# Kernel optimization log

Hardware: AMD Instinct MI355X
Metric: run time of the kernel (lower is better)

Reference implementation:

```python
import jax, jax.numpy as jnp
import numpy as np

TEMP = 0.05
EPS = 1e-8  # matches torch F.cosine_similarity eps default


def setup_inputs() -> dict:
    key = jax.random.key(0)
    k1, k2 = jax.random.split(key)
    B, L, H = 2048, 13, 768
    cls = jax.random.normal(k1, (B, H), dtype=jnp.float32)
    hidden = jax.random.normal(k2, (B, L, H), dtype=jnp.float32)
    return {"cls": cls, "hidden": hidden}


def _normalize(x, axis=-1):
    n = jnp.sqrt(jnp.sum(x * x, axis=axis, keepdims=True))
    return x / jnp.maximum(n, EPS)


def reference(cls, hidden):
    B, L, H = hidden.shape
    cn = _normalize(cls)            # [B, H]
    hn = _normalize(hidden)         # [B, L, H]

    # exp(cos(cls_i, hidden_{i,k}) / temp) -- aligned (diagonal) similarities
    sim_ci_hik = jnp.exp(jnp.einsum('id,ild->il', cn, hn) / TEMP)  # [B, L]

    # exp(cos(cls_i, hidden_{m,n}) / temp) -- all pairs, flattened (m,n)-major
    sim_ci_hmn = jnp.exp(jnp.einsum('id,mnd->imn', cn, hn) / TEMP)  # [B, B, L]
    sim_flat = sim_ci_hmn.reshape(B, B * L)                         # [B, B*L]

    # faithful to original: mask tiles (1 - eye(B)) L times along columns,
    # i.e. zeroes columns c with c % B == i (layout quirk of the source code)
    hmn_mask = jnp.tile(1.0 - jnp.eye(B, dtype=sim_flat.dtype), (1, L))  # [B, B*L]
    s = jnp.sum(sim_flat * hmn_mask, axis=1)                             # [B]

    loss = jnp.mean(-jnp.log(sim_ci_hik) + jnp.log(sim_ci_hik + s[:, None]))
    return loss
```

## Files before the change

### kernel.cpp

```cpp
#include <hip/hip_runtime.h>
#include <cstdint>
#include <cstddef>

#define B_    2048
#define L_    13
#define H_    768
#define NROW  (B_ * L_)
#define RTEMP 20.0f
#define NT    12
#define RS    768
#define NTILE 3328

typedef float f32x4 __attribute__((ext_vector_type(4)));
typedef long  i64x2 __attribute__((ext_vector_type(2)));

static __device__ __forceinline__ unsigned int f2e4m3(float f) {
  unsigned int u = __float_as_uint(f);
  unsigned int s = (u >> 24) & 0x80u;
  unsigned int ua = u & 0x7fffffffu;
  if (ua >= 0x43e80000u) return s | 0x7eu;
  if (ua < 0x3c800000u) {
    int m = (int)rintf(__uint_as_float(ua) * 512.0f);
    return s | (unsigned int)m;
  }
  unsigned int lsb = (ua >> 20) & 1u;
  unsigned int r = ua + 0x7ffffu + lsb;
  int Ee = (int)((r >> 23) & 0xffu) - 127;
  unsigned int mant = (r >> 20) & 7u;
  return s | (unsigned int)(((Ee + 7) << 3) | mant);
}

__device__ __forceinline__ void llds16(const void* g, void* l) {
  __builtin_amdgcn_global_load_lds(
      (const __attribute__((address_space(1))) void*)g,
      (__attribute__((address_space(3))) void*)l, 16, 0, 0);
}

#define BAR do { asm volatile("" ::: "memory");            \
    __builtin_amdgcn_s_barrier();                          \
    asm volatile("" ::: "memory"); } while (0)

#define OFF8(k) ((((k) >> 6) << 6) + (((((k) & 31) >> 3)) << 4) + ((((k) & 32) ? 8 : 0)) + ((k) & 7))

__global__ __launch_bounds__(256) void k_normalize(
    const float* __restrict__ cls, const float* __restrict__ hidden,
    unsigned char* __restrict__ cn8, unsigned char* __restrict__ hn8,
    float* __restrict__ S_all, float* __restrict__ out)
{
  if (blockIdx.x == 0) {
#pragma unroll
    for (int i = 0; i < 8; ++i) S_all[threadIdx.x * 8 + i] = 0.0f;
    if (threadIdx.x == 0) *out = 0.0f;
  }

  const int wid = threadIdx.x >> 6, lane = threadIdx.x & 63;
  const int row = blockIdx.x * 4 + wid;
  const float4* src; unsigned char* dst;
  if (row < B_) { src = (const float4*)(cls + (size_t)row * H_);           dst = cn8 + (size_t)row * RS; }
  else          { src = (const float4*)(hidden + (size_t)(row - B_) * H_); dst = hn8 + (size_t)(row - B_) * RS; }

  float4 x0 = src[lane], x1 = src[lane + 64], x2 = src[lane + 128];
  float ss = x0.x*x0.x + x0.y*x0.y + x0.z*x0.z + x0.w*x0.w
           + x1.x*x1.x + x1.y*x1.y + x1.z*x1.z + x1.w*x1.w
           + x2.x*x2.x + x2.y*x2.y + x2.z*x2.z + x2.w*x2.w;
#pragma unroll
  for (int m = 1; m < 64; m <<= 1) ss += __shfl_xor(ss, m);
  const float sc = 1.0f / fmaxf(sqrtf(ss), 1e-8f);

  const int k = lane * 4;
  unsigned int p0 = f2e4m3(x0.x*sc) | (f2e4m3(x0.y*sc) << 8) | (f2e4m3(x0.z*sc) << 16) | (f2e4m3(x0.w*sc) << 24);
  unsigned int p1 = f2e4m3(x1.x*sc) | (f2e4m3(x1.y*sc) << 8) | (f2e4m3(x1.z*sc) << 16) | (f2e4m3(x1.w*sc) << 24);
  unsigned int p2 = f2e4m3(x2.x*sc) | (f2e4m3(x2.y*sc) << 8) | (f2e4m3(x2.z*sc) << 16) | (f2e4m3(x2.w*sc) << 24);
  *(unsigned int*)(dst + OFF8(k))       = p0;
  *(unsigned int*)(dst + OFF8(k + 256)) = p1;
  *(unsigned int*)(dst + OFF8(k + 512)) = p2;
}

__global__ __launch_bounds__(256, 4) void k_gemm(
    const unsigned char* __restrict__ cn8,
    const unsigned char* __restrict__ hn8,
    float* __restrict__ S_all,
    float* __restrict__ alignedD)
{
  __shared__ __align__(16) char lds[40960];

  const int tid  = threadIdx.x;
  const int lane = tid & 63;
  const int wid  = tid >> 6;
  const int wm   = wid >> 1;
  const int wn   = wid & 1;
  const int fr   = lane & 15, q = lane >> 4, fr2 = (lane & 15) >> 1;

  const int swz  = ((q | ((fr & 1) << 2)) ^ (fr2 & 7)) << 4;
  const int offA = wm * 4096 + fr2 * 128 + swz;
  const int offB = wn * 4096 + fr2 * 128 + swz;

  const int slot_un = (tid & 7) ^ ((tid >> 3) & 7);
  const int srow = 2 * (tid >> 3) + (slot_un >> 2);
  const int scb  = (slot_un & 3) << 4;
  char* ldst = lds + tid * 16;

  const int tile = blockIdx.x;
  const int xcd  = tile & 7;
  const int idx  = tile >> 3;
  const int brow = (idx & 15) << 7;
  const int bcol = (xcd * 26 + (idx >> 4)) << 7;

  const char* gA = (const char*)cn8 + (size_t)(brow + srow) * RS + scb;
  const char* gB = (const char*)hn8 + (size_t)(bcol + srow) * RS + scb;

#define STAGE_A(sb, t) do {                                       \
    char* d_ = ldst + (sb);                                       \
    const char* a_ = gA + (t) * 64;                               \
    llds16(a_,           d_);                                     \
    llds16(a_ + 64 * RS, d_ + 4096);                              \
  } while (0)
#define STAGE_B(sb, t) do {                                       \
    char* d_ = ldst + (sb);                                       \
    const char* b_ = gB + (t) * 64;                               \
    llds16(b_,           d_);                                     \
    llds16(b_ + 64 * RS, d_ + 4096);                              \
  } while (0)

  STAGE_A(0, 0);
  STAGE_B(16384, 0);
  STAGE_B(16384 + 8192, 1);
  asm volatile("s_waitcnt vmcnt(2)" ::: "memory");
  BAR;

  f32x4 acc[4][4] = {};

  for (int t = 0; t < NT; ++t) {
    const char* bA = lds + (t & 1) * 8192;
    const char* bB = lds + 16384 + (t % 3) * 8192;

    i64x2 av[4], bv[4];
#pragma unroll
    for (int i = 0; i < 4; ++i) av[i] = *(const i64x2*)(bA + offA + i * 1024);
#pragma unroll
    for (int i = 0; i < 4; ++i) bv[i] = *(const i64x2*)(bB + offB + i * 1024);

    if (t + 1 < NT) STAGE_A(((t + 1) & 1) * 8192, t + 1);
    if (t + 2 < NT) STAGE_B(16384 + ((t + 2) % 3) * 8192, t + 2);

    __builtin_amdgcn_s_setprio(1);
#pragma unroll
    for (int mi = 0; mi < 4; ++mi)
#pragma unroll
      for (int ni = 0; ni < 4; ++ni)
        acc[mi][ni] = __builtin_amdgcn_mfma_f32_16x16x32_fp8_fp8(
            av[mi][0], bv[ni][0], acc[mi][ni], 0, 0, 0);
#pragma unroll
    for (int mi = 0; mi < 4; ++mi)
#pragma unroll
      for (int ni = 0; ni < 4; ++ni)
        acc[mi][ni] = __builtin_amdgcn_mfma_f32_16x16x32_fp8_fp8(
            av[mi][1], bv[ni][1], acc[mi][ni], 0, 0, 0);
    __builtin_amdgcn_s_setprio(0);

    if (t + 2 < NT)      { asm volatile("s_waitcnt vmcnt(2)" ::: "memory"); BAR; }
    else if (t + 1 < NT) { asm volatile("s_waitcnt vmcnt(0)" ::: "memory"); BAR; }
  }
#undef STAGE_A
#undef STAGE_B

  const int rowb = brow + wm * 64;
  const int colb = bcol + wn * 64;
#pragma unroll
  for (int mi = 0; mi < 4; ++mi) {
#pragma unroll
    for (int j = 0; j < 4; ++j) {
      const int grow = rowb + mi * 16 + q * 4 + j;
      float v = 0.f;
#pragma unroll
      for (int ni = 0; ni < 4; ++ni) {
        const int gcol = colb + ni * 16 + fr;
        const float a = acc[mi][ni][j];
        if ((unsigned)(gcol - grow * 13) < 13u) alignedD[gcol] = a;
        v += ((gcol & 2047) == grow) ? 0.f : __expf(RTEMP * a);
      }
      v += __shfl_xor(v, 1); v += __shfl_xor(v, 2);
      v += __shfl_xor(v, 4); v += __shfl_xor(v, 8);
      if (fr == 0) atomicAdd(&S_all[grow], v);
    }
  }
}

__global__ __launch_bounds__(256) void k_finalize(
    const float* __restrict__ S_all, const float* __restrict__ alignedD,
    float* __restrict__ out)
{
  const int i = blockIdx.x * 256 + threadIdx.x;
  const int lane = threadIdx.x & 63, wid = threadIdx.x >> 6;
  const float s = S_all[i];
  float accv = 0.f;
#pragma unroll
  for (int l = 0; l < L_; l++) {
    const float d = RTEMP * alignedD[i * L_ + l];
    accv += logf(__expf(d) + s) - d;
  }
#pragma unroll
  for (int m = 1; m < 64; m <<= 1) accv += __shfl_xor(accv, m);
  __shared__ float wsum[4];
  if (lane == 0) wsum[wid] = accv;
  __syncthreads();
  if (threadIdx.x == 0)
    atomicAdd(out, (wsum[0] + wsum[1] + wsum[2] + wsum[3]) * (1.0f / (float)(B_ * L_)));
}

extern "C" void kernel_launch(void* const* d_in, const int* in_sizes, int n_in,
                              void* d_out, int out_size, void* d_ws, size_t ws_size,
                              hipStream_t stream) {
  const float* cls    = (const float*)d_in[0];
  const float* hidden = (const float*)d_in[1];
  float* out = (float*)d_out;

  char* ws = (char*)d_ws;
  unsigned char* hn8 = (unsigned char*)ws;
  unsigned char* cn8 = (unsigned char*)(ws + (size_t)NROW * RS);
  float* S_all    = (float*)(ws + (size_t)NROW * RS + (size_t)B_ * RS);
  float* alignedD = (float*)(ws + (size_t)NROW * RS + (size_t)B_ * RS + B_ * sizeof(float));

  k_normalize<<<(B_ + NROW) / 4, 256, 0, stream>>>(cls, hidden, cn8, hn8, S_all, out);
  k_gemm<<<NTILE, 256, 0, stream>>>(cn8, hn8, S_all, alignedD);
  k_finalize<<<B_ / 256, 256, 0, stream>>>(S_all, alignedD, out);
}
```

Baseline: 92.15 us.

## Restructure FP8 GEMM main loop into triple-buffered pipeline with register prefetch

Replaces the asymmetric A-double/B-triple LDS buffering with a uniform triple buffer for both operands and a loop unrolled by two. The loop keeps two register fragment sets so LDS reads for the next K-step are issued before the MFMAs of the current one. The aim is to hide LDS read and global-to-LDS load latency behind matrix work. In exchange, LDS per block grows to 48 KB and the occupancy hint drops from 4 to 3 blocks per CU, and every step now waits for vmcnt(0).

```diff
diff --git a/kernel.cpp b/kernel.cpp
--- a/kernel.cpp
+++ b/kernel.cpp
@@ -39,6 +39,7 @@
 #define BAR do { asm volatile("" ::: "memory");            \
     __builtin_amdgcn_s_barrier();                          \
     asm volatile("" ::: "memory"); } while (0)
+#define WAITV0 asm volatile("s_waitcnt vmcnt(0)" ::: "memory")
 
 #define OFF8(k) ((((k) >> 6) << 6) + (((((k) & 31) >> 3)) << 4) + ((((k) & 32) ? 8 : 0)) + ((k) & 7))
 
@@ -76,13 +77,13 @@
   *(unsigned int*)(dst + OFF8(k + 512)) = p2;
 }
 
-__global__ __launch_bounds__(256, 4) void k_gemm(
+__global__ __launch_bounds__(256, 3) void k_gemm(
     const unsigned char* __restrict__ cn8,
     const unsigned char* __restrict__ hn8,
     float* __restrict__ S_all,
     float* __restrict__ alignedD)
 {
-  __shared__ __align__(16) char lds[40960];
+  __shared__ __align__(16) char lds[49152];
 
   const int tid  = threadIdx.x;
   const int lane = tid & 63;
@@ -98,7 +99,6 @@
   const int slot_un = (tid & 7) ^ ((tid >> 3) & 7);
   const int srow = 2 * (tid >> 3) + (slot_un >> 2);
   const int scb  = (slot_un & 3) << 4;
-  char* ldst = lds + tid * 16;
 
   const int tile = blockIdx.x;
   const int xcd  = tile & 7;
@@ -109,60 +109,84 @@
   const char* gA = (const char*)cn8 + (size_t)(brow + srow) * RS + scb;
   const char* gB = (const char*)hn8 + (size_t)(bcol + srow) * RS + scb;
 
-#define STAGE_A(sb, t) do {                                       \
-    char* d_ = ldst + (sb);                                       \
+  char* aCur = lds;          char* bCur = lds + 24576;
+  char* aNxt = lds + 8192;   char* bNxt = lds + 32768;
+  char* aWr  = lds + 16384;  char* bWr  = lds + 40960;
+
+#define STAGE(pa, pb, t) do {                                     \
     const char* a_ = gA + (t) * 64;                               \
-    llds16(a_,           d_);                                     \
-    llds16(a_ + 64 * RS, d_ + 4096);                              \
+    llds16(a_,           (pa) + tid * 16);                        \
+    llds16(a_ + 64 * RS, (pa) + 4096 + tid * 16);                 \
+    const char* b_ = gB + (t) * 64;                               \
+    llds16(b_,           (pb) + tid * 16);                        \
+    llds16(b_ + 64 * RS, (pb) + 4096 + tid * 16);                 \
   } while (0)
-#define STAGE_B(sb, t) do {                                       \
-    char* d_ = ldst + (sb);                                       \
-    const char* b_ = gB + (t) * 64;                               \
-    llds16(b_,           d_);                                     \
-    llds16(b_ + 64 * RS, d_ + 4096);                              \
+
+#define READSET(av, bv, pa, pb) do {                              \
+    _Pragma("unroll")                                             \
+    for (int i = 0; i < 4; ++i)                                   \
+      av[i] = *(const i64x2*)((pa) + offA + i * 1024);            \
+    _Pragma("unroll")                                             \
+    for (int i = 0; i < 4; ++i)                                   \
+      bv[i] = *(const i64x2*)((pb) + offB + i * 1024);            \
   } while (0)
 
-  STAGE_A(0, 0);
-  STAGE_B(16384, 0);
-  STAGE_B(16384 + 8192, 1);
-  asm volatile("s_waitcnt vmcnt(2)" ::: "memory");
+#define MFMAS(av, bv) do {                                        \
+    __builtin_amdgcn_s_setprio(1);                                \
+    _Pragma("unroll")                                             \
+    for (int mi = 0; mi < 4; ++mi)                                \
+      _Pragma("unroll")                                           \
+      for (int ni = 0; ni < 4; ++ni)                              \
+        acc[mi][ni] = __builtin_amdgcn_mfma_f32_16x16x32_fp8_fp8( \
+            av[mi][0], bv[ni][0], acc[mi][ni], 0, 0, 0);          \
+    _Pragma("unroll")                                             \
+    for (int mi = 0; mi < 4; ++mi)                                \
+      _Pragma("unroll")                                           \
+      for (int ni = 0; ni < 4; ++ni)                              \
+        acc[mi][ni] = __builtin_amdgcn_mfma_f32_16x16x32_fp8_fp8( \
+            av[mi][1], bv[ni][1], acc[mi][ni], 0, 0, 0);          \
+    __builtin_amdgcn_s_setprio(0);                                \
+  } while (0)
+
+#define ROTATE do { char* t_;                                     \
+    t_ = aCur; aCur = aNxt; aNxt = aWr; aWr = t_;                 \
+    t_ = bCur; bCur = bNxt; bNxt = bWr; bWr = t_; } while (0)
+
+  f32x4 acc[4][4] = {};
+  i64x2 a0[4], b0[4], a1[4], b1[4];
+
+  STAGE(aCur, bCur, 0);
+  WAITV0;
   BAR;
-
-  f32x4 acc[4][4] = {};
-
-  for (int t = 0; t < NT; ++t) {
-    const char* bA = lds + (t & 1) * 8192;
-    const char* bB = lds + 16384 + (t % 3) * 8192;
-
-    i64x2 av[4], bv[4];
-#pragma unroll
-    for (int i = 0; i < 4; ++i) av[i] = *(const i64x2*)(bA + offA + i * 1024);
-#pragma unroll
-    for (int i = 0; i < 4; ++i) bv[i] = *(const i64x2*)(bB + offB + i * 1024);
-
-    if (t + 1 < NT) STAGE_A(((t + 1) & 1) * 8192, t + 1);
-    if (t + 2 < NT) STAGE_B(16384 + ((t + 2) % 3) * 8192, t + 2);
-
-    __builtin_amdgcn_s_setprio(1);
-#pragma unroll
-    for (int mi = 0; mi < 4; ++mi)
-#pragma unroll
-      for (int ni = 0; ni < 4; ++ni)
-        acc[mi][ni] = __builtin_amdgcn_mfma_f32_16x16x32_fp8_fp8(
-            av[mi][0], bv[ni][0], acc[mi][ni], 0, 0, 0);
-#pragma unroll
-    for (int mi = 0; mi < 4; ++mi)
-#pragma unroll
-      for (int ni = 0; ni < 4; ++ni)
-        acc[mi][ni] = __builtin_amdgcn_mfma_f32_16x16x32_fp8_fp8(
-            av[mi][1], bv[ni][1], acc[mi][ni], 0, 0, 0);
-    __builtin_amdgcn_s_setprio(0);
-
-    if (t + 2 < NT)      { asm volatile("s_waitcnt vmcnt(2)" ::: "memory"); BAR; }
-    else if (t + 1 < NT) { asm volatile("s_waitcnt vmcnt(0)" ::: "memory"); BAR; }
-  }
-#undef STAGE_A
-#undef STAGE_B
+  READSET(a0, b0, aCur, bCur);
+  STAGE(aNxt, bNxt, 1);
+
+  for (int it = 0; it < 5; ++it) {
+    const int t = 2 * it;
+    WAITV0;
+    BAR;
+    READSET(a1, b1, aNxt, bNxt);
+    STAGE(aWr, bWr, t + 2);
+    MFMAS(a0, b0);
+    ROTATE;
+    WAITV0;
+    BAR;
+    READSET(a0, b0, aNxt, bNxt);
+    STAGE(aWr, bWr, t + 3);
+    MFMAS(a1, b1);
+    ROTATE;
+  }
+
+  WAITV0;
+  BAR;
+  READSET(a1, b1, aNxt, bNxt);
+  MFMAS(a0, b0);
+  MFMAS(a1, b1);
+
+#undef STAGE
+#undef READSET
+#undef MFMAS
+#undef ROTATE
 
   const int rowb = brow + wm * 64;
   const int colb = bcol + wn * 64;
```

Result: slower. 114.9 us (+24.6%).

## Restructure fp8 GEMM into a five-stage K=32 LDS ring with a new swizzle

Applied to the files above, without the earlier changes.

The GEMM main loop moves from a K-step of 64, with double-buffered A and triple-buffered B, to a K-step of 32. A and B now share a five-slot LDS ring that keeps up to four stages in flight, and the loop is fully unrolled with explicit vmcnt waits. The normalize kernel stops writing the permuted OFF8 fp8 layout, so a new XOR swizzle for LDS reads and staging addresses replaces it. The aim is deeper latency hiding of global-to-LDS loads. The cost is twice as many barriers and shorter 32-byte contiguous global segments per row.

```diff
diff --git a/kernel.cpp b/kernel.cpp
--- a/kernel.cpp
+++ b/kernel.cpp
@@ -7,12 +7,10 @@
 #define H_    768
 #define NROW  (B_ * L_)
 #define RTEMP 20.0f
-#define NT    12
 #define RS    768
 #define NTILE 3328
 
 typedef float f32x4 __attribute__((ext_vector_type(4)));
-typedef long  i64x2 __attribute__((ext_vector_type(2)));
 
 static __device__ __forceinline__ unsigned int f2e4m3(float f) {
   unsigned int u = __float_as_uint(f);
@@ -40,8 +38,6 @@
     __builtin_amdgcn_s_barrier();                          \
     asm volatile("" ::: "memory"); } while (0)
 
-#define OFF8(k) ((((k) >> 6) << 6) + (((((k) & 31) >> 3)) << 4) + ((((k) & 32) ? 8 : 0)) + ((k) & 7))
-
 __global__ __launch_bounds__(256) void k_normalize(
     const float* __restrict__ cls, const float* __restrict__ hidden,
     unsigned char* __restrict__ cn8, unsigned char* __restrict__ hn8,
@@ -71,9 +67,9 @@
   unsigned int p0 = f2e4m3(x0.x*sc) | (f2e4m3(x0.y*sc) << 8) | (f2e4m3(x0.z*sc) << 16) | (f2e4m3(x0.w*sc) << 24);
   unsigned int p1 = f2e4m3(x1.x*sc) | (f2e4m3(x1.y*sc) << 8) | (f2e4m3(x1.z*sc) << 16) | (f2e4m3(x1.w*sc) << 24);
   unsigned int p2 = f2e4m3(x2.x*sc) | (f2e4m3(x2.y*sc) << 8) | (f2e4m3(x2.z*sc) << 16) | (f2e4m3(x2.w*sc) << 24);
-  *(unsigned int*)(dst + OFF8(k))       = p0;
-  *(unsigned int*)(dst + OFF8(k + 256)) = p1;
-  *(unsigned int*)(dst + OFF8(k + 512)) = p2;
+  *(unsigned int*)(dst + k)       = p0;
+  *(unsigned int*)(dst + k + 256) = p1;
+  *(unsigned int*)(dst + k + 512) = p2;
 }
 
 __global__ __launch_bounds__(256, 4) void k_gemm(
@@ -89,16 +85,29 @@
   const int wid  = tid >> 6;
   const int wm   = wid >> 1;
   const int wn   = wid & 1;
-  const int fr   = lane & 15, q = lane >> 4, fr2 = (lane & 15) >> 1;
-
-  const int swz  = ((q | ((fr & 1) << 2)) ^ (fr2 & 7)) << 4;
-  const int offA = wm * 4096 + fr2 * 128 + swz;
-  const int offB = wn * 4096 + fr2 * 128 + swz;
-
-  const int slot_un = (tid & 7) ^ ((tid >> 3) & 7);
-  const int srow = 2 * (tid >> 3) + (slot_un >> 2);
-  const int scb  = (slot_un & 3) << 4;
-  char* ldst = lds + tid * 16;
+  const int fr   = lane & 15, q = lane >> 4;
+  const int l4   = fr >> 2, c3 = fr & 3;
+
+  int offA[4], offB[4];
+#pragma unroll
+  for (int mi = 0; mi < 4; ++mi) {
+    const int line = wm * 16 + mi * 4 + l4;
+    const int hkey = (mi * 2 + (l4 >> 1)) & 7;
+    const int u    = (c3 * 2 + (q >> 1)) ^ hkey;
+    offA[mi] = line * 128 + u * 16 + (q & 1) * 8;
+  }
+#pragma unroll
+  for (int ni = 0; ni < 4; ++ni) {
+    const int line = wn * 16 + ni * 4 + l4;
+    const int hkey = (ni * 2 + (l4 >> 1)) & 7;
+    const int u    = (c3 * 2 + (q >> 1)) ^ hkey;
+    offB[ni] = 4096 + line * 128 + u * 16 + (q & 1) * 8;
+  }
+
+  const int sline = tid >> 3, su = tid & 7;
+  const int sv    = su ^ ((sline >> 1) & 7);
+  const int srow  = sline * 4 + (sv >> 1);
+  const int skb   = (sv & 1) * 16;
 
   const int tile = blockIdx.x;
   const int xcd  = tile & 7;
@@ -106,63 +115,62 @@
   const int brow = (idx & 15) << 7;
   const int bcol = (xcd * 26 + (idx >> 4)) << 7;
 
-  const char* gA = (const char*)cn8 + (size_t)(brow + srow) * RS + scb;
-  const char* gB = (const char*)hn8 + (size_t)(bcol + srow) * RS + scb;
-
-#define STAGE_A(sb, t) do {                                       \
-    char* d_ = ldst + (sb);                                       \
-    const char* a_ = gA + (t) * 64;                               \
-    llds16(a_,           d_);                                     \
-    llds16(a_ + 64 * RS, d_ + 4096);                              \
+  const char* gA = (const char*)cn8 + (size_t)(brow + srow) * RS + skb;
+  const char* gB = (const char*)hn8 + (size_t)(bcol + srow) * RS + skb;
+  char* dA = lds + tid * 16;
+  char* dB = lds + 4096 + tid * 16;
+
+#define STAGE(slotidx, koff) do {                                 \
+    llds16(gA + (koff), dA + (slotidx) * 8192);                   \
+    llds16(gB + (koff), dB + (slotidx) * 8192);                   \
   } while (0)
-#define STAGE_B(sb, t) do {                                       \
-    char* d_ = ldst + (sb);                                       \
-    const char* b_ = gB + (t) * 64;                               \
-    llds16(b_,           d_);                                     \
-    llds16(b_ + 64 * RS, d_ + 4096);                              \
+
+  f32x4 acc[4][4] = {};
+
+#define DOSTEP(j, stagej, koff, wait) do {                        \
+    if (stagej) STAGE((j + 4) % 5, koff);                         \
+    const char* sb_ = lds + (j) * 8192;                           \
+    long av[4], bv[4];                                            \
+    _Pragma("unroll")                                             \
+    for (int i = 0; i < 4; ++i) av[i] = *(const long*)(sb_ + offA[i]); \
+    _Pragma("unroll")                                             \
+    for (int i = 0; i < 4; ++i) bv[i] = *(const long*)(sb_ + offB[i]); \
+    __builtin_amdgcn_s_setprio(1);                                \
+    _Pragma("unroll")                                             \
+    for (int mi = 0; mi < 4; ++mi)                                \
+      _Pragma("unroll")                                           \
+      for (int ni = 0; ni < 4; ++ni)                              \
+        acc[mi][ni] = __builtin_amdgcn_mfma_f32_16x16x32_fp8_fp8( \
+            av[mi], bv[ni], acc[mi][ni], 0, 0, 0);                \
+    __builtin_amdgcn_s_setprio(0);                                \
+    if (wait >= 0) {                                              \
+      if (wait == 6) asm volatile("s_waitcnt vmcnt(6)" ::: "memory"); \
+      else if (wait == 4) asm volatile("s_waitcnt vmcnt(4)" ::: "memory"); \
+      else if (wait == 2) asm volatile("s_waitcnt vmcnt(2)" ::: "memory"); \
+      else                asm volatile("s_waitcnt vmcnt(0)" ::: "memory"); \
+      BAR;                                                        \
+    }                                                             \
   } while (0)
 
-  STAGE_A(0, 0);
-  STAGE_B(16384, 0);
-  STAGE_B(16384 + 8192, 1);
-  asm volatile("s_waitcnt vmcnt(2)" ::: "memory");
+  STAGE(0, 0); STAGE(1, 32); STAGE(2, 64); STAGE(3, 96);
+  asm volatile("s_waitcnt vmcnt(6)" ::: "memory");
   BAR;
 
-  f32x4 acc[4][4] = {};
-
-  for (int t = 0; t < NT; ++t) {
-    const char* bA = lds + (t & 1) * 8192;
-    const char* bB = lds + 16384 + (t % 3) * 8192;
-
-    i64x2 av[4], bv[4];
-#pragma unroll
-    for (int i = 0; i < 4; ++i) av[i] = *(const i64x2*)(bA + offA + i * 1024);
-#pragma unroll
-    for (int i = 0; i < 4; ++i) bv[i] = *(const i64x2*)(bB + offB + i * 1024);
-
-    if (t + 1 < NT) STAGE_A(((t + 1) & 1) * 8192, t + 1);
-    if (t + 2 < NT) STAGE_B(16384 + ((t + 2) % 3) * 8192, t + 2);
-
-    __builtin_amdgcn_s_setprio(1);
-#pragma unroll
-    for (int mi = 0; mi < 4; ++mi)
-#pragma unroll
-      for (int ni = 0; ni < 4; ++ni)
-        acc[mi][ni] = __builtin_amdgcn_mfma_f32_16x16x32_fp8_fp8(
-            av[mi][0], bv[ni][0], acc[mi][ni], 0, 0, 0);
-#pragma unroll
-    for (int mi = 0; mi < 4; ++mi)
-#pragma unroll
-      for (int ni = 0; ni < 4; ++ni)
-        acc[mi][ni] = __builtin_amdgcn_mfma_f32_16x16x32_fp8_fp8(
-            av[mi][1], bv[ni][1], acc[mi][ni], 0, 0, 0);
-    __builtin_amdgcn_s_setprio(0);
-
-    if (t + 2 < NT)      { asm volatile("s_waitcnt vmcnt(2)" ::: "memory"); BAR; }
-    else if (t + 1 < NT) { asm volatile("s_waitcnt vmcnt(0)" ::: "memory"); BAR; }
-  }
-#undef STAGE_A
-#undef STAGE_B
+  for (int it = 0; it < 4; ++it) {
+    DOSTEP(0, true, 4 * 32, 6);
+    DOSTEP(1, true, 5 * 32, 6);
+    DOSTEP(2, true, 6 * 32, 6);
+    DOSTEP(3, true, 7 * 32, 6);
+    DOSTEP(4, true, 8 * 32, 6);
+    gA += 160; gB += 160;
+  }
+  DOSTEP(0, false, 0, 4);
+  DOSTEP(1, false, 0, 2);
+  DOSTEP(2, false, 0, 0);
+  DOSTEP(3, false, 0, -1);
+
+#undef DOSTEP
+#undef STAGE
 
   const int rowb = brow + wm * 64;
   const int colb = bcol + wn * 64;
```

New measurement: 123.6 us. 1.34x slower.

## Switch FP8 GEMM to 32x32x64 scaled MFMA with plain row layout

Applied to the files above, without the earlier changes.

Replaces the 16x16x32 fp8 MFMA tiles with the gfx950 mfma_scale 32x32x64 f8f6f4 instruction, using unit scales, so each wave issues 4 larger MFMAs per K-step instead of 32 small ones. The normalize kernel now writes fp8 rows in natural order instead of the interleaved OFF8 layout. LDS read offsets are recomputed with a new XOR swizzle for the 32-row fragments, and the epilogue is adapted to the 32x32 accumulator lane mapping with a wider shuffle reduction. The aim is higher matrix-core throughput and fewer LDS reads. The risk is that the new fragment layout or the scale operands do not match the instruction's expected operand format.

```diff
diff --git a/kernel.cpp b/kernel.cpp
--- a/kernel.cpp
+++ b/kernel.cpp
@@ -10,9 +10,11 @@
 #define NT    12
 #define RS    768
 #define NTILE 3328
-
-typedef float f32x4 __attribute__((ext_vector_type(4)));
-typedef long  i64x2 __attribute__((ext_vector_type(2)));
+#define SC1   0x7F7F7F7F
+
+typedef int   i32x4  __attribute__((ext_vector_type(4)));
+typedef int   i32x8  __attribute__((ext_vector_type(8)));
+typedef float f32x16 __attribute__((ext_vector_type(16)));
 
 static __device__ __forceinline__ unsigned int f2e4m3(float f) {
   unsigned int u = __float_as_uint(f);
@@ -40,8 +42,6 @@
     __builtin_amdgcn_s_barrier();                          \
     asm volatile("" ::: "memory"); } while (0)
 
-#define OFF8(k) ((((k) >> 6) << 6) + (((((k) & 31) >> 3)) << 4) + ((((k) & 32) ? 8 : 0)) + ((k) & 7))
-
 __global__ __launch_bounds__(256) void k_normalize(
     const float* __restrict__ cls, const float* __restrict__ hidden,
     unsigned char* __restrict__ cn8, unsigned char* __restrict__ hn8,
@@ -71,9 +71,9 @@
   unsigned int p0 = f2e4m3(x0.x*sc) | (f2e4m3(x0.y*sc) << 8) | (f2e4m3(x0.z*sc) << 16) | (f2e4m3(x0.w*sc) << 24);
   unsigned int p1 = f2e4m3(x1.x*sc) | (f2e4m3(x1.y*sc) << 8) | (f2e4m3(x1.z*sc) << 16) | (f2e4m3(x1.w*sc) << 24);
   unsigned int p2 = f2e4m3(x2.x*sc) | (f2e4m3(x2.y*sc) << 8) | (f2e4m3(x2.z*sc) << 16) | (f2e4m3(x2.w*sc) << 24);
-  *(unsigned int*)(dst + OFF8(k))       = p0;
-  *(unsigned int*)(dst + OFF8(k + 256)) = p1;
-  *(unsigned int*)(dst + OFF8(k + 512)) = p2;
+  *(unsigned int*)(dst + k)       = p0;
+  *(unsigned int*)(dst + k + 256) = p1;
+  *(unsigned int*)(dst + k + 512) = p2;
 }
 
 __global__ __launch_bounds__(256, 4) void k_gemm(
@@ -89,16 +89,31 @@
   const int wid  = tid >> 6;
   const int wm   = wid >> 1;
   const int wn   = wid & 1;
-  const int fr   = lane & 15, q = lane >> 4, fr2 = (lane & 15) >> 1;
-
-  const int swz  = ((q | ((fr & 1) << 2)) ^ (fr2 & 7)) << 4;
-  const int offA = wm * 4096 + fr2 * 128 + swz;
-  const int offB = wn * 4096 + fr2 * 128 + swz;
+  const int rr   = lane & 31;
+  const int h    = lane >> 5;
+
+  const int keyq = (rr >> 1) & 7;
+  int offA[2][2], offB[2][2];
+#pragma unroll
+  for (int mi = 0; mi < 2; ++mi)
+#pragma unroll
+    for (int j = 0; j < 2; ++j) {
+      const int line = wm * 32 + mi * 16 + (rr >> 1);
+      const int v    = (rr & 1) * 4 + 2 * h + j;
+      offA[mi][j] = line * 128 + ((v ^ keyq) << 4);
+    }
+#pragma unroll
+  for (int ni = 0; ni < 2; ++ni)
+#pragma unroll
+    for (int j = 0; j < 2; ++j) {
+      const int line = wn * 32 + ni * 16 + (rr >> 1);
+      const int v    = (rr & 1) * 4 + 2 * h + j;
+      offB[ni][j] = line * 128 + ((v ^ keyq) << 4);
+    }
 
   const int slot_un = (tid & 7) ^ ((tid >> 3) & 7);
   const int srow = 2 * (tid >> 3) + (slot_un >> 2);
   const int scb  = (slot_un & 3) << 4;
-  char* ldst = lds + tid * 16;
 
   const int tile = blockIdx.x;
   const int xcd  = tile & 7;
@@ -108,18 +123,17 @@
 
   const char* gA = (const char*)cn8 + (size_t)(brow + srow) * RS + scb;
   const char* gB = (const char*)hn8 + (size_t)(bcol + srow) * RS + scb;
+  char* ldst = lds + tid * 16;
 
 #define STAGE_A(sb, t) do {                                       \
-    char* d_ = ldst + (sb);                                       \
     const char* a_ = gA + (t) * 64;                               \
-    llds16(a_,           d_);                                     \
-    llds16(a_ + 64 * RS, d_ + 4096);                              \
+    llds16(a_,           ldst + (sb));                            \
+    llds16(a_ + 64 * RS, ldst + (sb) + 4096);                     \
   } while (0)
 #define STAGE_B(sb, t) do {                                       \
-    char* d_ = ldst + (sb);                                       \
     const char* b_ = gB + (t) * 64;                               \
-    llds16(b_,           d_);                                     \
-    llds16(b_ + 64 * RS, d_ + 4096);                              \
+    llds16(b_,           ldst + (sb));                            \
+    llds16(b_ + 64 * RS, ldst + (sb) + 4096);                     \
   } while (0)
 
   STAGE_A(0, 0);
@@ -128,34 +142,36 @@
   asm volatile("s_waitcnt vmcnt(2)" ::: "memory");
   BAR;
 
-  f32x4 acc[4][4] = {};
+  f32x16 acc[2][2] = {};
 
   for (int t = 0; t < NT; ++t) {
     const char* bA = lds + (t & 1) * 8192;
     const char* bB = lds + 16384 + (t % 3) * 8192;
 
-    i64x2 av[4], bv[4];
-#pragma unroll
-    for (int i = 0; i < 4; ++i) av[i] = *(const i64x2*)(bA + offA + i * 1024);
-#pragma unroll
-    for (int i = 0; i < 4; ++i) bv[i] = *(const i64x2*)(bB + offB + i * 1024);
+    i32x8 av[2], bv[2];
+#pragma unroll
+    for (int mi = 0; mi < 2; ++mi) {
+      i32x4 lo = *(const i32x4*)(bA + offA[mi][0]);
+      i32x4 hi = *(const i32x4*)(bA + offA[mi][1]);
+      av[mi] = __builtin_shufflevector(lo, hi, 0, 1, 2, 3, 4, 5, 6, 7);
+    }
+#pragma unroll
+    for (int ni = 0; ni < 2; ++ni) {
+      i32x4 lo = *(const i32x4*)(bB + offB[ni][0]);
+      i32x4 hi = *(const i32x4*)(bB + offB[ni][1]);
+      bv[ni] = __builtin_shufflevector(lo, hi, 0, 1, 2, 3, 4, 5, 6, 7);
+    }
 
     if (t + 1 < NT) STAGE_A(((t + 1) & 1) * 8192, t + 1);
     if (t + 2 < NT) STAGE_B(16384 + ((t + 2) % 3) * 8192, t + 2);
 
     __builtin_amdgcn_s_setprio(1);
 #pragma unroll
-    for (int mi = 0; mi < 4; ++mi)
-#pragma unroll
-      for (int ni = 0; ni < 4; ++ni)
-        acc[mi][ni] = __builtin_amdgcn_mfma_f32_16x16x32_fp8_fp8(
-            av[mi][0], bv[ni][0], acc[mi][ni], 0, 0, 0);
-#pragma unroll
-    for (int mi = 0; mi < 4; ++mi)
-#pragma unroll
-      for (int ni = 0; ni < 4; ++ni)
-        acc[mi][ni] = __builtin_amdgcn_mfma_f32_16x16x32_fp8_fp8(
-            av[mi][1], bv[ni][1], acc[mi][ni], 0, 0, 0);
+    for (int mi = 0; mi < 2; ++mi)
+#pragma unroll
+      for (int ni = 0; ni < 2; ++ni)
+        acc[mi][ni] = __builtin_amdgcn_mfma_scale_f32_32x32x64_f8f6f4(
+            av[mi], bv[ni], acc[mi][ni], 0, 0, 0, SC1, 0, SC1);
     __builtin_amdgcn_s_setprio(0);
 
     if (t + 2 < NT)      { asm volatile("s_waitcnt vmcnt(2)" ::: "memory"); BAR; }
@@ -167,21 +183,21 @@
   const int rowb = brow + wm * 64;
   const int colb = bcol + wn * 64;
 #pragma unroll
-  for (int mi = 0; mi < 4; ++mi) {
-#pragma unroll
-    for (int j = 0; j < 4; ++j) {
-      const int grow = rowb + mi * 16 + q * 4 + j;
+  for (int mi = 0; mi < 2; ++mi) {
+#pragma unroll
+    for (int j = 0; j < 16; ++j) {
+      const int grow = rowb + mi * 32 + (j & 3) + 8 * (j >> 2) + 4 * h;
       float v = 0.f;
 #pragma unroll
-      for (int ni = 0; ni < 4; ++ni) {
-        const int gcol = colb + ni * 16 + fr;
+      for (int ni = 0; ni < 2; ++ni) {
+        const int gcol = colb + ni * 32 + rr;
         const float a = acc[mi][ni][j];
         if ((unsigned)(gcol - grow * 13) < 13u) alignedD[gcol] = a;
         v += ((gcol & 2047) == grow) ? 0.f : __expf(RTEMP * a);
       }
       v += __shfl_xor(v, 1); v += __shfl_xor(v, 2);
-      v += __shfl_xor(v, 4); v += __shfl_xor(v, 8);
-      if (fr == 0) atomicAdd(&S_all[grow], v);
+      v += __shfl_xor(v, 4); v += __shfl_xor(v, 8); v += __shfl_xor(v, 16);
+      if (rr == 0) atomicAdd(&S_all[grow], v);
     }
   }
 }
```

Measured after the change: 357.4 us. +287.9%, slower.
